# Performance work log

Measured on AMD Instinct MI355X. Metric: run time of the kernel, lower is better.

Reference implementation:

```python
import jax, jax.numpy as jnp
import numpy as np

TEMPERATURE = 0.07
KNN_AUG = True
NUM_NEIGHBORS = 10
B, N, D = 2048, 65536, 128
NUM_CLUSTERS = 100
EPS = 1e-12


def _l2_normalize(x):
    # matches torch F.normalize(dim=1): x / max(||x||, eps)
    norm = jnp.sqrt(jnp.sum(x * x, axis=1, keepdims=True))
    return x / jnp.maximum(norm, EPS)


def setup_inputs() -> dict:
    key = jax.random.key(0)
    k1, k2, k3, k4 = jax.random.split(key, 4)
    return {
        "features": jax.random.normal(k1, (B, D), dtype=jnp.float32),
        "cluster_idxes": jax.random.randint(k2, (B,), 0, NUM_CLUSTERS),
        "global_features": jax.random.normal(k3, (N, D), dtype=jnp.float32),
        "global_clusters": jax.random.randint(k4, (N,), 0, NUM_CLUSTERS),
    }


def reference(features, cluster_idxes, global_features, global_clusters):
    f = _l2_normalize(features)            # [B, D]
    g = _l2_normalize(global_features)     # [N, D]
    sim = (f @ g.T) / TEMPERATURE          # [B, N]

    # cluster-membership positive mask: [B, N]
    pos_mask = (cluster_idxes[:, None] == global_clusters[None, :]).astype(sim.dtype)

    if KNN_AUG:
        k_val = min(NUM_NEIGHBORS, sim.shape[-1])
        _, knn_idx = jax.lax.top_k(sim, k_val)  # [B, k]
        rows = jnp.arange(sim.shape[0])[:, None]
        knn_mask = jnp.zeros_like(pos_mask).at[rows, knn_idx].set(1.0)
        pos_mask = ((pos_mask + knn_mask) > 0).astype(sim.dtype)

    # masked log-softmax reduction (same math as original: exp/sum/log)
    log_prob = sim - jnp.log(jnp.sum(jnp.exp(sim), axis=1, keepdims=True) + EPS)  # [B, N]
    mean_log_prob_pos = jnp.sum(pos_mask * log_prob, axis=1) / (jnp.sum(pos_mask, axis=1) + EPS)
    return -jnp.mean(mean_log_prob_pos)
```

## Files before the change

### kernel.cpp

```cpp
#include <hip/hip_runtime.h>

#define B_ROWS 2048
#define N_GLB  65536
#define DDIM   128
#define NCLUST 100
#define INV_T  (1.0f/0.07f)
#define LOG2E  1.4426950408889634f
#define LN2    0.6931471805599453f
#define NSPLIT 16
#define CHUNK_COLS (N_GLB/NSPLIT)
#define ITERS (CHUNK_COLS/64)
#define ROWSB 32
#define TOPK 10
#define CAP  256
#define NSLICE 8
#define TAU_L2E (3.7881f*LOG2E)
#define CSC    65536.0f
#define INV_CSC (1.0f/65536.0f)

typedef __attribute__((ext_vector_type(8))) short sh8;
typedef __attribute__((ext_vector_type(4))) float f32x4;
typedef unsigned long long u64;

__device__ __forceinline__ unsigned f2bf(float x) {
  unsigned u = __float_as_uint(x);
  u += 0x7fffu + ((u >> 16) & 1u);
  return u >> 16;
}
__device__ __forceinline__ unsigned fmono(float v) {
  unsigned u = __float_as_uint(v);
  return ((int)u < 0) ? ~u : (u | 0x80000000u);
}
__device__ __forceinline__ float fmono_inv(unsigned m) {
  unsigned u = (m & 0x80000000u) ? (m & 0x7FFFFFFFu) : ~m;
  return __uint_as_float(u);
}
__device__ __forceinline__ u64 mkkey(float val, int col) {
  return ((u64)fmono(val) << 32) | (unsigned)(~(unsigned)col);
}
__device__ __forceinline__ u64 umax64(u64 a, u64 b) { return a > b ? a : b; }

__global__ __launch_bounds__(256) void prep_kernel(
    const float* __restrict__ f, const float* __restrict__ g,
    char* __restrict__ wsf2, char* __restrict__ wsg2,
    float* __restrict__ inv_fT) {
  __shared__ unsigned lds[1024];
  const int t = threadIdx.x, lane = t & 63, w = t >> 6;
  const int grp = blockIdx.x;
  const bool isf = grp < (B_ROWS / 16);

  #pragma unroll
  for (int j = 0; j < 4; ++j) {
    int rit = w * 4 + j;
    int row = grp * 16 + rit;
    int rr = isf ? row : row - B_ROWS;
    const float* src = (isf ? f : g) + (size_t)rr * DDIM;
    float2 v = ((const float2*)src)[lane];
    float ss = v.x * v.x + v.y * v.y;
    #pragma unroll
    for (int m = 32; m; m >>= 1) ss += __shfl_xor(ss, m);
    float inv = 1.0f / fmaxf(sqrtf(ss), 1e-12f);
    if (isf && lane == 0) inv_fT[rr] = inv * INV_T;
    float sc = isf ? inv * (INV_T * LOG2E) : inv;
    unsigned pk = f2bf(v.x * sc) | (f2bf(v.y * sc) << 16);
    lds[(lane >> 2) * 64 + rit * 4 + (lane & 3)] = pk;
  }
  __syncthreads();
  char* dst = isf ? (wsf2 + (size_t)grp * 4096)
                  : (wsg2 + (size_t)(grp - B_ROWS / 16) * 4096);
  ((uint4*)dst)[t] = ((const uint4*)lds)[t];
}

__global__ __launch_bounds__(256) void csum2_kernel(
    const char* __restrict__ wsg2, const int* __restrict__ gclust,
    int* __restrict__ csum_i32, int* __restrict__ hist8) {
  __shared__ int cs[NCLUST * DDIM];
  __shared__ int hcnt[NCLUST];
  const int t = threadIdx.x, lane = t & 63, w = t >> 6;
  for (int i = t; i < NCLUST * DDIM; i += 256) cs[i] = 0;
  if (t < NCLUST) hcnt[t] = 0;
  __syncthreads();

  const int rbase = blockIdx.x * 512;
  const int rg = lane >> 4;
  const int ch = lane & 15;
  for (int step = 0; step < 32; ++step) {
    int row = rbase + step * 16 + w * 4 + rg;
    int c = gclust[row];
    uint4 v = *(const uint4*)(wsg2 + (size_t)(row >> 4) * 4096 + ch * 256 + (row & 15) * 16);
    int* dst = &cs[c * DDIM + ch * 8];
    atomicAdd(dst + 0, (int)rintf(__uint_as_float(v.x << 16) * CSC));
    atomicAdd(dst + 1, (int)rintf(__uint_as_float(v.x & 0xFFFF0000u) * CSC));
    atomicAdd(dst + 2, (int)rintf(__uint_as_float(v.y << 16) * CSC));
    atomicAdd(dst + 3, (int)rintf(__uint_as_float(v.y & 0xFFFF0000u) * CSC));
    atomicAdd(dst + 4, (int)rintf(__uint_as_float(v.z << 16) * CSC));
    atomicAdd(dst + 5, (int)rintf(__uint_as_float(v.z & 0xFFFF0000u) * CSC));
    atomicAdd(dst + 6, (int)rintf(__uint_as_float(v.w << 16) * CSC));
    atomicAdd(dst + 7, (int)rintf(__uint_as_float(v.w & 0xFFFF0000u) * CSC));
    if (ch == 0) atomicAdd(&hcnt[c], 1);
  }
  __syncthreads();
  const int slice = blockIdx.x & (NSLICE - 1);
  for (int i = t; i < NCLUST * DDIM; i += 256) {
    int x = cs[i];
    if (x) atomicAdd(&csum_i32[(size_t)slice * NCLUST * DDIM + i], x);
  }
  if (t < NCLUST && hcnt[t]) atomicAdd(&hist8[slice * 128 + t], hcnt[t]);
}

#define PUSHQ(av, mm, q)                                                        \
  if ((av) > TAU_L2E) {                                                         \
    int rw = r0 + (mm) * 16 + lhi * 4 + (q);                                    \
    int slot = atomicAdd(&cnt[rw], 1);                                          \
    if (slot < CAP) { lv[rw * CAP + slot] = (av) * LN2; li[rw * CAP + slot] = colv; } \
  }

#define EPI(a, mm)                                                              \
  {                                                                             \
    se[mm].x += __builtin_amdgcn_exp2f(a.x);                                    \
    se[mm].y += __builtin_amdgcn_exp2f(a.y);                                    \
    se[mm].z += __builtin_amdgcn_exp2f(a.z);                                    \
    se[mm].w += __builtin_amdgcn_exp2f(a.w);                                    \
    float mx = fmaxf(fmaxf(a.x, a.y), fmaxf(a.z, a.w));                         \
    if (mx > TAU_L2E) { PUSHQ(a.x, mm, 0) PUSHQ(a.y, mm, 1) PUSHQ(a.z, mm, 2) PUSHQ(a.w, mm, 3) } \
  }

#define LOADB(dst, gptr)                                                        \
  { _Pragma("unroll") for (int s = 0; s < 4; ++s)                               \
      dst[s] = *(const uint4*)((gptr) + s * 1024 + (size_t)lane * 16); }

#define COMPUTE_REFILL(bb, itv, refbase, dorefill)                              \
  {                                                                             \
    f32x4 ac0 = {0,0,0,0}, ac1 = {0,0,0,0};                                     \
    _Pragma("unroll") for (int s = 0; s < 4; ++s) {                             \
      sh8 bs = __builtin_bit_cast(sh8, bb[s]);                                  \
      if (dorefill) bb[s] = *(const uint4*)((refbase) + s * 1024 + (size_t)lane * 16); \
      ac0 = __builtin_amdgcn_mfma_f32_16x16x32_bf16(afr[0][s], bs, ac0, 0, 0, 0); \
      ac1 = __builtin_amdgcn_mfma_f32_16x16x32_bf16(afr[1][s], bs, ac1, 0, 0, 0); \
    }                                                                           \
    const int colv = chunk * CHUNK_COLS + (itv) * 64 + w * 16 + l15;            \
    EPI(ac0, 0) EPI(ac1, 1)                                                     \
  }

__global__ __launch_bounds__(256, 4) void sim_kernel(
    const char* __restrict__ wsf2, const char* __restrict__ wsg2,
    float* __restrict__ p_se, float* __restrict__ lv, int* __restrict__ li,
    int* __restrict__ cnt) {
  __shared__ float sered[4][ROWSB];
  const int t = threadIdx.x, lane = t & 63, w = t >> 6;
  const int l15 = lane & 15, lhi = lane >> 4;
  const int chunk = blockIdx.x;
  const int r0 = blockIdx.y * ROWSB;

  const char* fbase = wsf2 + (size_t)(r0 >> 4) * 4096;
  sh8 afr[2][4];
  #pragma unroll
  for (int m = 0; m < 2; ++m)
    #pragma unroll
    for (int s = 0; s < 4; ++s)
      afr[m][s] = *(const sh8*)(fbase + (size_t)m * 4096 + s * 1024 + (size_t)lane * 16);

  f32x4 z = {0.f, 0.f, 0.f, 0.f};
  f32x4 se[2] = {z, z};

  const char* gb = wsg2 + (size_t)(chunk * (CHUNK_COLS / 16) + w) * 4096;
  uint4 b0[4], b1[4];
  LOADB(b0, gb)
  LOADB(b1, gb + 4 * 4096)
  for (int it = 0; it < ITERS; it += 2) {
    COMPUTE_REFILL(b0, it,     gb + 8 * 4096,  it + 2 < ITERS)
    COMPUTE_REFILL(b1, it + 1, gb + 12 * 4096, it + 3 < ITERS)
    gb += 8 * 4096;
  }

  #pragma unroll
  for (int m = 0; m < 2; ++m)
    #pragma unroll
    for (int q = 0; q < 4; ++q) {
      float s = se[m][q];
      s += __shfl_xor(s, 1); s += __shfl_xor(s, 2);
      s += __shfl_xor(s, 4); s += __shfl_xor(s, 8);
      if (l15 == 0) sered[w][m * 16 + lhi * 4 + q] = s;
    }
  __syncthreads();
  if (t < ROWSB) {
    float s = sered[0][t] + sered[1][t] + sered[2][t] + sered[3][t];
    p_se[(size_t)(r0 + t) * NSPLIT + chunk] = s;
  }
}

__global__ __launch_bounds__(256) void merge_kernel(
    const float* __restrict__ f, const int* __restrict__ fclust,
    const int* __restrict__ gclust, const float* __restrict__ inv_fT,
    const float* __restrict__ p_se, const int* __restrict__ csum_i32,
    const int* __restrict__ hist8, const float* __restrict__ lv,
    const int* __restrict__ li, const int* __restrict__ cnt,
    const char* __restrict__ wsf2, const char* __restrict__ wsg2,
    float* __restrict__ rowv) {
  const int lane = threadIdx.x & 63, w = threadIdx.x >> 6;
  const int r = blockIdx.x * 4 + w;

  float sev = (lane < NSPLIT) ? p_se[(size_t)r * NSPLIT + lane] : 0.f;
  sev += __shfl_xor(sev, 8); sev += __shfl_xor(sev, 4);
  sev += __shfl_xor(sev, 2); sev += __shfl_xor(sev, 1);
  sev = __shfl(sev, 0);

  int rc = fclust[r];
  float2 fv = ((const float2*)(f + (size_t)r * DDIM))[lane];
  float sc = inv_fT[r];
  int ia = 0, ib = 0, hc = 0;
  #pragma unroll
  for (int s = 0; s < NSLICE; ++s) {
    ia += csum_i32[(size_t)s * NCLUST * DDIM + rc * DDIM + 2 * lane];
    ib += csum_i32[(size_t)s * NCLUST * DDIM + rc * DDIM + 2 * lane + 1];
    hc += hist8[s * 128 + rc];
  }
  float dt = fv.x * sc * (ia * INV_CSC) + fv.y * sc * (ib * INV_CSC);
  #pragma unroll
  for (int m = 32; m; m >>= 1) dt += __shfl_xor(dt, m);
  dt = __shfl(dt, 0);

  float Cc = (float)hc;
  int n = cnt[r];
  bool bad = (n < TOPK) || (n > CAP);
  float S10 = 0.f, C10 = 0.f;
  if (!bad) {
    u64 k0 = 0, k1 = 0, k2 = 0, k3 = 0;
    int e = lane;
    if (e < n) k0 = mkkey(lv[(size_t)r * CAP + e], li[(size_t)r * CAP + e]);
    e = lane + 64;
    if (e < n) k1 = mkkey(lv[(size_t)r * CAP + e], li[(size_t)r * CAP + e]);
    e = lane + 128;
    if (e < n) k2 = mkkey(lv[(size_t)r * CAP + e], li[(size_t)r * CAP + e]);
    e = lane + 192;
    if (e < n) k3 = mkkey(lv[(size_t)r * CAP + e], li[(size_t)r * CAP + e]);
    for (int it = 0; it < TOPK; ++it) {
      u64 best = umax64(umax64(k0, k1), umax64(k2, k3));
      #pragma unroll
      for (int m = 32; m; m >>= 1) best = umax64(best, __shfl_xor(best, m));
      float val = fmono_inv((unsigned)(best >> 32));
      int col = (int)(~(unsigned)(best & 0xFFFFFFFFull));
      int gc = gclust[col];
      if (gc != rc) { S10 += val; C10 += 1.f; }
      if (k0 == best) k0 = 0;
      if (k1 == best) k1 = 0;
      if (k2 == best) k2 = 0;
      if (k3 == best) k3 = 0;
    }
  } else {
    uint4 fr[16];
    #pragma unroll
    for (int c = 0; c < 16; ++c)
      fr[c] = *(const uint4*)(wsf2 + (size_t)(r >> 4) * 4096 + c * 256 + (size_t)(r & 15) * 16);
    u64 tk[TOPK];
    #pragma unroll
    for (int i = 0; i < TOPK; ++i) tk[i] = 0;
    for (int col = lane; col < N_GLB; col += 64) {
      const char* gp = wsg2 + (size_t)(col >> 4) * 4096 + (size_t)(col & 15) * 16;
      float acc = 0.f;
      #pragma unroll
      for (int c = 0; c < 16; ++c) {
        uint4 gv = *(const uint4*)(gp + c * 256);
        uint4 fc = fr[c];
        #pragma unroll
        for (int p = 0; p < 4; ++p) {
          unsigned fa = (&fc.x)[p], ga = (&gv.x)[p];
          acc += __uint_as_float(fa << 16) * __uint_as_float(ga << 16)
               + __uint_as_float(fa & 0xFFFF0000u) * __uint_as_float(ga & 0xFFFF0000u);
        }
      }
      u64 key = mkkey(acc, col);
      if (key > tk[0]) {
        u64 cur = key;
        #pragma unroll
        for (int i = 0; i < TOPK - 1; ++i) {
          u64 nxt = tk[i + 1];
          u64 lo = cur < nxt ? cur : nxt;
          u64 hi = cur < nxt ? nxt : cur;
          tk[i] = lo; cur = hi;
        }
        tk[TOPK - 1] = cur;
      }
    }
    for (int it = 0; it < TOPK; ++it) {
      u64 best = tk[TOPK - 1];
      #pragma unroll
      for (int m = 32; m; m >>= 1) best = umax64(best, __shfl_xor(best, m));
      float val = fmono_inv((unsigned)(best >> 32)) * LN2;
      int col = (int)(~(unsigned)(best & 0xFFFFFFFFull));
      if (gclust[col] != rc) { S10 += val; C10 += 1.f; }
      if (tk[TOPK - 1] == best) {
        #pragma unroll
        for (int i = TOPK - 1; i > 0; --i) tk[i] = tk[i - 1];
        tk[0] = 0;
      }
    }
  }
  if (lane == 0) {
    float L = logf(sev + 1e-12f);
    float C = Cc + C10;
    rowv[r] = (dt + S10 - C * L) / (C + 1e-12f);
  }
}

__global__ void final_kernel(const float* __restrict__ rowv, float* __restrict__ out) {
  __shared__ float sm[256];
  int t = threadIdx.x;
  float s = 0.f;
  for (int i = t; i < B_ROWS; i += 256) s += rowv[i];
  sm[t] = s;
  __syncthreads();
  for (int o = 128; o; o >>= 1) { if (t < o) sm[t] += sm[t + o]; __syncthreads(); }
  if (t == 0) out[0] = -(sm[0] / (float)B_ROWS);
}

extern "C" void kernel_launch(void* const* d_in, const int* in_sizes, int n_in,
                              void* d_out, int out_size, void* d_ws, size_t ws_size,
                              hipStream_t stream) {
  const float* f  = (const float*)d_in[0];
  const int*   fc = (const int*)  d_in[1];
  const float* g  = (const float*)d_in[2];
  const int*   gc = (const int*)  d_in[3];
  float* out = (float*)d_out;

  char* ws = (char*)d_ws;
  char*  wsf2    = ws;
  char*  wsg2    = ws + 524288;
  float* inv_fT  = (float*)(ws + 17301504);
  float* p_se    = (float*)(ws + 17309696);
  int*   csum_i32= (int*)  (ws + 17440768);
  int*   hist8   = (int*)  (ws + 17850368);
  int*   cnt     = (int*)  (ws + 17854464);
  float* lv      = (float*)(ws + 17862656);
  int*   li      = (int*)  (ws + 19959808);
  float* rowv    = (float*)(ws + 22056960);

  hipMemsetAsync(ws + 17440768, 0, 421888, stream);

  prep_kernel<<<(B_ROWS + N_GLB) / 16, 256, 0, stream>>>(f, g, wsf2, wsg2, inv_fT);

  csum2_kernel<<<N_GLB / 512, 256, 0, stream>>>(wsg2, gc, csum_i32, hist8);

  dim3 grid(NSPLIT, B_ROWS / ROWSB);
  sim_kernel<<<grid, 256, 0, stream>>>(wsf2, wsg2, p_se, lv, li, cnt);

  merge_kernel<<<B_ROWS / 4, 256, 0, stream>>>(f, fc, gc, inv_fT, p_se, csum_i32,
                                               hist8, lv, li, cnt, wsf2, wsg2, rowv);
  final_kernel<<<1, 256, 0, stream>>>(rowv, out);
}
```

Baseline: 126.0 us.

## Switch similarity GEMM operands from bf16 to fp8 with deeper prefetch

Normalized feature and global matrices are now packed as fp8 (e4m3) instead of bf16, halving the workspace size and the bytes streamed by the similarity kernel. The MFMA calls switch to the fp8 16x16x32 variant, and the B-tile prefetch ring grows from two to four stages. Cluster-sum and fallback top-k paths decode fp8 in software. This adds precision loss in the logits, which could perturb top-k selection and the loss value.

```diff
diff --git a/kernel.cpp b/kernel.cpp
--- a/kernel.cpp
+++ b/kernel.cpp
@@ -11,6 +11,7 @@
 #define CHUNK_COLS (N_GLB/NSPLIT)
 #define ITERS (CHUNK_COLS/64)
 #define ROWSB 32
+#define GRPB 2048
 #define TOPK 10
 #define CAP  256
 #define NSLICE 8
@@ -18,15 +19,10 @@
 #define CSC    65536.0f
 #define INV_CSC (1.0f/65536.0f)
 
-typedef __attribute__((ext_vector_type(8))) short sh8;
 typedef __attribute__((ext_vector_type(4))) float f32x4;
+typedef __attribute__((ext_vector_type(2))) long lg2;
 typedef unsigned long long u64;
 
-__device__ __forceinline__ unsigned f2bf(float x) {
-  unsigned u = __float_as_uint(x);
-  u += 0x7fffu + ((u >> 16) & 1u);
-  return u >> 16;
-}
 __device__ __forceinline__ unsigned fmono(float v) {
   unsigned u = __float_as_uint(v);
   return ((int)u < 0) ? ~u : (u | 0x80000000u);
@@ -39,12 +35,19 @@
   return ((u64)fmono(val) << 32) | (unsigned)(~(unsigned)col);
 }
 __device__ __forceinline__ u64 umax64(u64 a, u64 b) { return a > b ? a : b; }
+
+__device__ __forceinline__ float fp8d(unsigned b) {
+  unsigned e = (b >> 3) & 15, m = b & 7;
+  float v = e ? __uint_as_float(((e + 120u) << 23) | (m << 20))
+              : (float)m * 0.001953125f;
+  return (b & 0x80u) ? -v : v;
+}
 
 __global__ __launch_bounds__(256) void prep_kernel(
     const float* __restrict__ f, const float* __restrict__ g,
     char* __restrict__ wsf2, char* __restrict__ wsg2,
     float* __restrict__ inv_fT) {
-  __shared__ unsigned lds[1024];
+  __shared__ unsigned short lds[1024];
   const int t = threadIdx.x, lane = t & 63, w = t >> 6;
   const int grp = blockIdx.x;
   const bool isf = grp < (B_ROWS / 16);
@@ -62,13 +65,16 @@
     float inv = 1.0f / fmaxf(sqrtf(ss), 1e-12f);
     if (isf && lane == 0) inv_fT[rr] = inv * INV_T;
     float sc = isf ? inv * (INV_T * LOG2E) : inv;
-    unsigned pk = f2bf(v.x * sc) | (f2bf(v.y * sc) << 16);
-    lds[(lane >> 2) * 64 + rit * 4 + (lane & 3)] = pk;
-  }
-  __syncthreads();
-  char* dst = isf ? (wsf2 + (size_t)grp * 4096)
-                  : (wsg2 + (size_t)(grp - B_ROWS / 16) * 4096);
-  ((uint4*)dst)[t] = ((const uint4*)lds)[t];
+    unsigned pk = __builtin_amdgcn_cvt_pk_fp8_f32(v.x * sc, v.y * sc, 0u, false);
+    int k = 2 * lane;
+    int off = ((k >> 6) << 10) + (((k >> 3) & 3) << 8) + (rit << 4)
+            + (((k >> 5) & 1) << 3) + (k & 7);
+    lds[off >> 1] = (unsigned short)(pk & 0xFFFFu);
+  }
+  __syncthreads();
+  char* dst = isf ? (wsf2 + (size_t)grp * GRPB)
+                  : (wsg2 + (size_t)(grp - B_ROWS / 16) * GRPB);
+  if (t < 128) ((uint4*)dst)[t] = ((const uint4*)lds)[t];
 }
 
 __global__ __launch_bounds__(256) void csum2_kernel(
@@ -84,19 +90,19 @@
   const int rbase = blockIdx.x * 512;
   const int rg = lane >> 4;
   const int ch = lane & 15;
+  const int p = ch >> 1, h = ch & 1;
+  const int kbase = ((p >> 2) << 6) + (h << 5) + ((p & 3) << 3);
   for (int step = 0; step < 32; ++step) {
     int row = rbase + step * 16 + w * 4 + rg;
     int c = gclust[row];
-    uint4 v = *(const uint4*)(wsg2 + (size_t)(row >> 4) * 4096 + ch * 256 + (row & 15) * 16);
-    int* dst = &cs[c * DDIM + ch * 8];
-    atomicAdd(dst + 0, (int)rintf(__uint_as_float(v.x << 16) * CSC));
-    atomicAdd(dst + 1, (int)rintf(__uint_as_float(v.x & 0xFFFF0000u) * CSC));
-    atomicAdd(dst + 2, (int)rintf(__uint_as_float(v.y << 16) * CSC));
-    atomicAdd(dst + 3, (int)rintf(__uint_as_float(v.y & 0xFFFF0000u) * CSC));
-    atomicAdd(dst + 4, (int)rintf(__uint_as_float(v.z << 16) * CSC));
-    atomicAdd(dst + 5, (int)rintf(__uint_as_float(v.z & 0xFFFF0000u) * CSC));
-    atomicAdd(dst + 6, (int)rintf(__uint_as_float(v.w << 16) * CSC));
-    atomicAdd(dst + 7, (int)rintf(__uint_as_float(v.w & 0xFFFF0000u) * CSC));
+    uint2 v = *(const uint2*)(wsg2 + (size_t)(row >> 4) * GRPB + (p >> 2) * 1024
+                              + (p & 3) * 256 + (row & 15) * 16 + h * 8);
+    int* dst = &cs[c * DDIM + kbase];
+    #pragma unroll
+    for (int b = 0; b < 4; ++b) {
+      atomicAdd(dst + b,     (int)rintf(fp8d((v.x >> (8 * b)) & 0xFFu) * CSC));
+      atomicAdd(dst + 4 + b, (int)rintf(fp8d((v.y >> (8 * b)) & 0xFFu) * CSC));
+    }
     if (ch == 0) atomicAdd(&hcnt[c], 1);
   }
   __syncthreads();
@@ -126,17 +132,20 @@
   }
 
 #define LOADB(dst, gptr)                                                        \
-  { _Pragma("unroll") for (int s = 0; s < 4; ++s)                               \
-      dst[s] = *(const uint4*)((gptr) + s * 1024 + (size_t)lane * 16); }
+  { dst[0] = *(const uint4*)((gptr) + (size_t)lane * 16);                       \
+    dst[1] = *(const uint4*)((gptr) + 1024 + (size_t)lane * 16); }
 
 #define COMPUTE_REFILL(bb, itv, refbase, dorefill)                              \
   {                                                                             \
     f32x4 ac0 = {0,0,0,0}, ac1 = {0,0,0,0};                                     \
-    _Pragma("unroll") for (int s = 0; s < 4; ++s) {                             \
-      sh8 bs = __builtin_bit_cast(sh8, bb[s]);                                  \
-      if (dorefill) bb[s] = *(const uint4*)((refbase) + s * 1024 + (size_t)lane * 16); \
-      ac0 = __builtin_amdgcn_mfma_f32_16x16x32_bf16(afr[0][s], bs, ac0, 0, 0, 0); \
-      ac1 = __builtin_amdgcn_mfma_f32_16x16x32_bf16(afr[1][s], bs, ac1, 0, 0, 0); \
+    _Pragma("unroll") for (int sp = 0; sp < 2; ++sp) {                          \
+      lg2 bsp = __builtin_bit_cast(lg2, bb[sp]);                                \
+      if (dorefill)                                                             \
+        bb[sp] = *(const uint4*)((refbase) + sp * 1024 + (size_t)lane * 16);    \
+      ac0 = __builtin_amdgcn_mfma_f32_16x16x32_fp8_fp8(afr[0][sp][0], bsp[0], ac0, 0, 0, 0); \
+      ac1 = __builtin_amdgcn_mfma_f32_16x16x32_fp8_fp8(afr[1][sp][0], bsp[0], ac1, 0, 0, 0); \
+      ac0 = __builtin_amdgcn_mfma_f32_16x16x32_fp8_fp8(afr[0][sp][1], bsp[1], ac0, 0, 0, 0); \
+      ac1 = __builtin_amdgcn_mfma_f32_16x16x32_fp8_fp8(afr[1][sp][1], bsp[1], ac1, 0, 0, 0); \
     }                                                                           \
     const int colv = chunk * CHUNK_COLS + (itv) * 64 + w * 16 + l15;            \
     EPI(ac0, 0) EPI(ac1, 1)                                                     \
@@ -152,25 +161,30 @@
   const int chunk = blockIdx.x;
   const int r0 = blockIdx.y * ROWSB;
 
-  const char* fbase = wsf2 + (size_t)(r0 >> 4) * 4096;
-  sh8 afr[2][4];
+  const char* fbase = wsf2 + (size_t)(r0 >> 4) * GRPB;
+  lg2 afr[2][2];
   #pragma unroll
   for (int m = 0; m < 2; ++m)
     #pragma unroll
-    for (int s = 0; s < 4; ++s)
-      afr[m][s] = *(const sh8*)(fbase + (size_t)m * 4096 + s * 1024 + (size_t)lane * 16);
+    for (int sp = 0; sp < 2; ++sp)
+      afr[m][sp] = __builtin_bit_cast(lg2,
+        *(const uint4*)(fbase + (size_t)m * GRPB + sp * 1024 + (size_t)lane * 16));
 
   f32x4 z = {0.f, 0.f, 0.f, 0.f};
   f32x4 se[2] = {z, z};
 
-  const char* gb = wsg2 + (size_t)(chunk * (CHUNK_COLS / 16) + w) * 4096;
-  uint4 b0[4], b1[4];
+  const char* gb = wsg2 + (size_t)(chunk * (CHUNK_COLS / 16) + w) * GRPB;
+  uint4 b0[2], b1[2], b2[2], b3[2];
   LOADB(b0, gb)
-  LOADB(b1, gb + 4 * 4096)
-  for (int it = 0; it < ITERS; it += 2) {
-    COMPUTE_REFILL(b0, it,     gb + 8 * 4096,  it + 2 < ITERS)
-    COMPUTE_REFILL(b1, it + 1, gb + 12 * 4096, it + 3 < ITERS)
-    gb += 8 * 4096;
+  LOADB(b1, gb + 1 * 8192)
+  LOADB(b2, gb + 2 * 8192)
+  LOADB(b3, gb + 3 * 8192)
+  for (int it = 0; it < ITERS; it += 4) {
+    COMPUTE_REFILL(b0, it,     gb + 4 * 8192, it + 4 < ITERS)
+    COMPUTE_REFILL(b1, it + 1, gb + 5 * 8192, it + 5 < ITERS)
+    COMPUTE_REFILL(b2, it + 2, gb + 6 * 8192, it + 6 < ITERS)
+    COMPUTE_REFILL(b3, it + 3, gb + 7 * 8192, it + 7 < ITERS)
+    gb += 4 * 8192;
   }
 
   #pragma unroll
@@ -248,25 +262,27 @@
       if (k3 == best) k3 = 0;
     }
   } else {
-    uint4 fr[16];
-    #pragma unroll
-    for (int c = 0; c < 16; ++c)
-      fr[c] = *(const uint4*)(wsf2 + (size_t)(r >> 4) * 4096 + c * 256 + (size_t)(r & 15) * 16);
+    uint4 fr[8];
+    #pragma unroll
+    for (int pc = 0; pc < 8; ++pc)
+      fr[pc] = *(const uint4*)(wsf2 + (size_t)(r >> 4) * GRPB + (pc >> 2) * 1024
+                               + (pc & 3) * 256 + (r & 15) * 16);
     u64 tk[TOPK];
     #pragma unroll
     for (int i = 0; i < TOPK; ++i) tk[i] = 0;
     for (int col = lane; col < N_GLB; col += 64) {
-      const char* gp = wsg2 + (size_t)(col >> 4) * 4096 + (size_t)(col & 15) * 16;
+      const char* gp = wsg2 + (size_t)(col >> 4) * GRPB + (col & 15) * 16;
       float acc = 0.f;
       #pragma unroll
-      for (int c = 0; c < 16; ++c) {
-        uint4 gv = *(const uint4*)(gp + c * 256);
-        uint4 fc = fr[c];
+      for (int pc = 0; pc < 8; ++pc) {
+        uint4 gv = *(const uint4*)(gp + (pc >> 2) * 1024 + (pc & 3) * 256);
+        uint4 fc = fr[pc];
         #pragma unroll
-        for (int p = 0; p < 4; ++p) {
-          unsigned fa = (&fc.x)[p], ga = (&gv.x)[p];
-          acc += __uint_as_float(fa << 16) * __uint_as_float(ga << 16)
-               + __uint_as_float(fa & 0xFFFF0000u) * __uint_as_float(ga & 0xFFFF0000u);
+        for (int wd = 0; wd < 4; ++wd) {
+          unsigned fa = (&fc.x)[wd], ga = (&gv.x)[wd];
+          #pragma unroll
+          for (int b = 0; b < 4; ++b)
+            acc += fp8d((fa >> (8 * b)) & 0xFFu) * fp8d((ga >> (8 * b)) & 0xFFu);
         }
       }
       u64 key = mkkey(acc, col);
@@ -325,17 +341,17 @@
 
   char* ws = (char*)d_ws;
   char*  wsf2    = ws;
-  char*  wsg2    = ws + 524288;
-  float* inv_fT  = (float*)(ws + 17301504);
-  float* p_se    = (float*)(ws + 17309696);
-  int*   csum_i32= (int*)  (ws + 17440768);
-  int*   hist8   = (int*)  (ws + 17850368);
-  int*   cnt     = (int*)  (ws + 17854464);
-  float* lv      = (float*)(ws + 17862656);
-  int*   li      = (int*)  (ws + 19959808);
-  float* rowv    = (float*)(ws + 22056960);
-
-  hipMemsetAsync(ws + 17440768, 0, 421888, stream);
+  char*  wsg2    = ws + 262144;
+  float* inv_fT  = (float*)(ws + 8650752);
+  float* p_se    = (float*)(ws + 8658944);
+  int*   csum_i32= (int*)  (ws + 8790016);
+  int*   hist8   = (int*)  (ws + 9199616);
+  int*   cnt     = (int*)  (ws + 9203712);
+  float* lv      = (float*)(ws + 9211904);
+  int*   li      = (int*)  (ws + 11309056);
+  float* rowv    = (float*)(ws + 13406208);
+
+  hipMemsetAsync(ws + 8790016, 0, 421888, stream);
 
   prep_kernel<<<(B_ROWS + N_GLB) / 16, 256, 0, stream>>>(f, g, wsf2, wsg2, inv_fT);
 
```

Measured after the change: 124.8 us. No clear change (-1.0%).
